# Kernel optimization log

Hardware: AMD Instinct MI355X
Metric: run time of the kernel (lower is better)

## Reference

```python
import jax, jax.numpy as jnp
import numpy as np

N_NODES = 100000
N_EDGES = 1600000
N_GRAPHS = 512
F_IN, HID, EMB = 256, 64, 2


def gcn_layer(h, src, dst, W, b, n_nodes):
    # PyG GCNConv: h' = D^{-1/2} (A + I) D^{-1/2} (h W) + b
    h = h @ W  # [N, out]
    loop = jnp.arange(n_nodes)
    s = jnp.concatenate([src, loop])
    d = jnp.concatenate([dst, loop])
    deg = jax.ops.segment_sum(jnp.ones_like(d, dtype=h.dtype), d, num_segments=n_nodes)
    dinv = jnp.where(deg > 0, jax.lax.rsqrt(deg), 0.0)
    norm = dinv[s] * dinv[d]  # [E+N]
    msg = h[s] * norm[:, None]  # gather + scale
    return jax.ops.segment_sum(msg, d, num_segments=n_nodes) + b


def setup_inputs() -> dict:
    key = jax.random.key(0)
    k1, k2, k3, k4, k5, k6 = jax.random.split(key, 6)
    x = jax.random.normal(k1, (N_NODES, F_IN), dtype=jnp.float32)
    edge_index = jax.random.randint(k2, (2, N_EDGES), 0, N_NODES, dtype=jnp.int64)
    batch = jnp.sort(jax.random.randint(k3, (N_NODES,), 0, N_GRAPHS, dtype=jnp.int64))
    # Glorot-ish init for layer weights
    W1 = jax.random.normal(k4, (F_IN, HID), dtype=jnp.float32) / np.sqrt(F_IN)
    b1 = jnp.zeros((HID,), dtype=jnp.float32)
    W2 = jax.random.normal(k5, (HID, EMB), dtype=jnp.float32) / np.sqrt(HID)
    b2 = jnp.zeros((EMB,), dtype=jnp.float32)
    return {"x": x, "edge_index": edge_index, "batch": batch,
            "W1": W1, "b1": b1, "W2": W2, "b2": b2}


def reference(x, edge_index, batch, W1, b1, W2, b2):
    n = x.shape[0]
    src, dst = edge_index[0], edge_index[1]
    h = gcn_layer(x, src, dst, W1, b1, n)
    h = jax.nn.relu(h)
    h = gcn_layer(h, src, dst, W2, b2, n)
    # global_mean_pool over graph ids
    sums = jax.ops.segment_sum(h, batch, num_segments=N_GRAPHS)
    cnts = jax.ops.segment_sum(jnp.ones((n,), dtype=h.dtype), batch, num_segments=N_GRAPHS)
    return sums / jnp.maximum(cnts, 1.0)[:, None]
```

## Files before the change

kernel.cpp:

```cpp
#include <hip/hip_runtime.h>
#include <hip/hip_bf16.h>

#define FIN 256
#define HID 64
#define EMB 2
#define BKB 9
#define BKSZ 512
#define MAXBK 256
#define NBLK 256

typedef __bf16 bf16x8 __attribute__((ext_vector_type(8)));
typedef float  f32x16 __attribute__((ext_vector_type(16)));

static __device__ __forceinline__ unsigned short f2bf(float f) {
    union { float f; unsigned int u; } v; v.f = f;
    unsigned int u = v.u;
    unsigned int r = (u + 0x7fffu + ((u >> 16) & 1u)) >> 16;
    return (unsigned short)r;
}
static __device__ __forceinline__ float bf2f(unsigned short h) {
    union { unsigned int u; float f; } v; v.u = ((unsigned int)h) << 16;
    return v.f;
}

__global__ void zero_i_kernel(int* __restrict__ p, long n) {
    long i = (long)blockIdx.x * blockDim.x + threadIdx.x;
    if (i < n) p[i] = 0;
}

__global__ void scan1_kernel(const int* __restrict__ cnt, int* __restrict__ offs,
                             int* __restrict__ bsums, int M) {
    __shared__ int s[256];
    int tid = threadIdx.x;
    int i = blockIdx.x * 256 + tid;
    int v = (i < M) ? cnt[i] : 0;
    s[tid] = v;
    __syncthreads();
    for (int off = 1; off < 256; off <<= 1) {
        int t = (tid >= off) ? s[tid - off] : 0;
        __syncthreads();
        s[tid] += t;
        __syncthreads();
    }
    if (i < M) offs[i + 1] = s[tid];
    if (tid == 255) bsums[blockIdx.x] = s[255];
    if (i == 0) offs[0] = 0;
}

__global__ void scan2_kernel(int* __restrict__ bsums, int NB) {
    __shared__ int s[512];
    int tid = threadIdx.x;
    s[tid] = (tid < NB) ? bsums[tid] : 0;
    __syncthreads();
    for (int off = 1; off < 512; off <<= 1) {
        int t = (tid >= off) ? s[tid - off] : 0;
        __syncthreads();
        s[tid] += t;
        __syncthreads();
    }
    if (tid < NB) bsums[tid] = s[tid];
}

__global__ void scan3_kernel(int* __restrict__ offs, const int* __restrict__ bsums, int M) {
    int i = blockIdx.x * 256 + threadIdx.x;
    if (i < M && blockIdx.x > 0) offs[i + 1] += bsums[blockIdx.x - 1];
}

__global__ __launch_bounds__(256) void bin_hist_kernel(
        const int* __restrict__ dst, int* __restrict__ counts, int E, int chunk, int NBK) {
    __shared__ int hist[MAXBK];
    int tid = threadIdx.x;
    for (int b = tid; b < NBK; b += 256) hist[b] = 0;
    __syncthreads();
    int e0 = blockIdx.x * chunk, e1 = min(e0 + chunk, E);
    for (int i = e0 + tid; i < e1; i += 256) atomicAdd(&hist[dst[i] >> BKB], 1);
    __syncthreads();
    for (int b = tid; b < NBK; b += 256) counts[b * gridDim.x + blockIdx.x] = hist[b];
}

__global__ __launch_bounds__(256) void bin_scatter_kernel(
        const int* __restrict__ src, const int* __restrict__ dst,
        const int* __restrict__ offs, unsigned* __restrict__ ebuf,
        int E, int chunk, int NBK) {
    __shared__ int cur[MAXBK];
    int tid = threadIdx.x;
    for (int b = tid; b < NBK; b += 256) cur[b] = offs[b * gridDim.x + blockIdx.x];
    __syncthreads();
    int e0 = blockIdx.x * chunk, e1 = min(e0 + chunk, E);
    for (int i = e0 + tid; i < e1; i += 256) {
        int s = src[i], d = dst[i];
        int b = d >> BKB;
        int pos = atomicAdd(&cur[b], 1);
        ebuf[pos] = ((unsigned)s << BKB) | (unsigned)(d & (BKSZ - 1));
    }
}

__global__ __launch_bounds__(256) void build_kernel(
        const unsigned* __restrict__ ebuf, const int* __restrict__ offs,
        int* __restrict__ rowptr, float* __restrict__ dinv, int* __restrict__ csr,
        int N, int E) {
    __shared__ int hist[BKSZ];
    __shared__ int scanb[256];
    __shared__ int cur[BKSZ];
    const int b = blockIdx.x, tid = threadIdx.x;
    const int r0 = offs[b * NBLK];
    const int r1 = offs[(b + 1) * NBLK];
    const int nb0 = b * BKSZ;

    hist[tid] = 0; hist[tid + 256] = 0;
    __syncthreads();
    for (int i = r0 + tid; i < r1; i += 256)
        atomicAdd(&hist[ebuf[i] & (BKSZ - 1u)], 1);
    __syncthreads();

    int h0 = hist[2 * tid], h1 = hist[2 * tid + 1];
    if (nb0 + 2 * tid < N)     dinv[nb0 + 2 * tid]     = rsqrtf((float)h0 + 1.f);
    if (nb0 + 2 * tid + 1 < N) dinv[nb0 + 2 * tid + 1] = rsqrtf((float)h1 + 1.f);
    scanb[tid] = h0 + h1;
    __syncthreads();
    for (int off = 1; off < 256; off <<= 1) {
        int t = (tid >= off) ? scanb[tid - off] : 0;
        __syncthreads();
        scanb[tid] += t;
        __syncthreads();
    }
    int base0 = scanb[tid] - (h0 + h1);
    int o0 = base0, o1 = base0 + h0;
    cur[2 * tid] = o0; cur[2 * tid + 1] = o1;
    if (nb0 + 2 * tid < N)     rowptr[nb0 + 2 * tid]     = r0 + o0;
    if (nb0 + 2 * tid + 1 < N) rowptr[nb0 + 2 * tid + 1] = r0 + o1;
    if (nb0 + BKSZ >= N && tid == 0) rowptr[N] = E;
    __syncthreads();
    for (int i = r0 + tid; i < r1; i += 256) {
        unsigned u = ebuf[i];
        int loc = (int)(u & (BKSZ - 1u));
        int p = atomicAdd(&cur[loc], 1);
        csr[r0 + p] = (int)(u >> BKB);
    }
}

__global__ __launch_bounds__(256) void gemm1_kernel(
        const float* __restrict__ x, const float* __restrict__ W,
        const float* __restrict__ dinv, unsigned short* __restrict__ h1b, int N) {
    __shared__ __align__(16) __bf16 A_hi[2 * 4 * 64 * 8];
    __shared__ __align__(16) __bf16 A_lo[2 * 4 * 64 * 8];
    __shared__ __align__(16) __bf16 B_hi[2 * 4 * 64 * 8];
    __shared__ __align__(16) __bf16 B_lo[2 * 4 * 64 * 8];

    const int tid = threadIdx.x;
    const int base = blockIdx.x * 64;
    const int w = tid >> 6;
    const int l = tid & 63;
    const int mg = w >> 1, ng = w & 1;

    f32x16 acc = {};

    const int r  = tid & 63;
    const int ks = tid >> 6;
    const int rl = r & 31, rh = r >> 5;

    for (int ch = 0; ch < 4; ++ch) {
        const int ck0 = ch * 64;
        __syncthreads();
        {
            int row = base + r;
            float f[16];
            if (row < N) {
                const float* xp = &x[(size_t)row * FIN + ck0 + ks * 16];
                float4 v0 = *(const float4*)(xp + 0);
                float4 v1 = *(const float4*)(xp + 4);
                float4 v2 = *(const float4*)(xp + 8);
                float4 v3 = *(const float4*)(xp + 12);
                f[0]=v0.x; f[1]=v0.y; f[2]=v0.z; f[3]=v0.w;
                f[4]=v1.x; f[5]=v1.y; f[6]=v1.z; f[7]=v1.w;
                f[8]=v2.x; f[9]=v2.y; f[10]=v2.z; f[11]=v2.w;
                f[12]=v3.x; f[13]=v3.y; f[14]=v3.z; f[15]=v3.w;
            } else {
                #pragma unroll
                for (int q = 0; q < 16; ++q) f[q] = 0.f;
            }
            bf16x8 ha, hb, la, lb;
            #pragma unroll
            for (int q = 0; q < 8; ++q) {
                __bf16 h0 = (__bf16)f[q];
                ha[q] = h0; la[q] = (__bf16)(f[q] - (float)h0);
                __bf16 h1v = (__bf16)f[q + 8];
                hb[q] = h1v; lb[q] = (__bf16)(f[q + 8] - (float)h1v);
            }
            int ra = ((rh * 4 + ks) * 64 + rl) * 8;
            int rb = ((rh * 4 + ks) * 64 + 32 + rl) * 8;
            *(bf16x8*)&A_hi[ra] = ha; *(bf16x8*)&A_hi[rb] = hb;
            *(bf16x8*)&A_lo[ra] = la; *(bf16x8*)&A_lo[rb] = lb;
        }
        {
            const float* wp = &W[(size_t)(ck0 + ks * 16) * HID + r];
            float f[16];
            #pragma unroll
            for (int q = 0; q < 16; ++q) f[q] = wp[q * HID];
            bf16x8 ha, hb, la, lb;
            #pragma unroll
            for (int q = 0; q < 8; ++q) {
                __bf16 h0 = (__bf16)f[q];
                ha[q] = h0; la[q] = (__bf16)(f[q] - (float)h0);
                __bf16 h1v = (__bf16)f[q + 8];
                hb[q] = h1v; lb[q] = (__bf16)(f[q + 8] - (float)h1v);
            }
            int ra = ((rh * 4 + ks) * 64 + rl) * 8;
            int rb = ((rh * 4 + ks) * 64 + 32 + rl) * 8;
            *(bf16x8*)&B_hi[ra] = ha; *(bf16x8*)&B_hi[rb] = hb;
            *(bf16x8*)&B_lo[ra] = la; *(bf16x8*)&B_lo[rb] = lb;
        }
        __syncthreads();

        #pragma unroll
        for (int s = 0; s < 4; ++s) {
            bf16x8 a_h = *(const bf16x8*)&A_hi[((mg * 4 + s) * 64 + l) * 8];
            bf16x8 a_l = *(const bf16x8*)&A_lo[((mg * 4 + s) * 64 + l) * 8];
            bf16x8 b_h = *(const bf16x8*)&B_hi[((ng * 4 + s) * 64 + l) * 8];
            bf16x8 b_l = *(const bf16x8*)&B_lo[((ng * 4 + s) * 64 + l) * 8];
            acc = __builtin_amdgcn_mfma_f32_32x32x16_bf16(a_h, b_h, acc, 0, 0, 0);
            acc = __builtin_amdgcn_mfma_f32_32x32x16_bf16(a_h, b_l, acc, 0, 0, 0);
            acc = __builtin_amdgcn_mfma_f32_32x32x16_bf16(a_l, b_h, acc, 0, 0, 0);
        }
    }

    const int col = l & 31;
    const int rbase = 4 * (l >> 5);
    #pragma unroll
    for (int reg = 0; reg < 16; ++reg) {
        int row = (reg & 3) + 8 * (reg >> 2) + rbase;
        int node = base + mg * 32 + row;
        if (node < N)
            h1b[(size_t)node * HID + ng * 32 + col] = f2bf(acc[reg] * dinv[node]);
    }
}

__global__ __launch_bounds__(256) void agg1_layer2_kernel(
        const int* __restrict__ rowptr, const int* __restrict__ csr,
        const unsigned short* __restrict__ h1b,
        const float* __restrict__ dinv, const float* __restrict__ b1,
        const float* __restrict__ W2, float* __restrict__ h2, int N) {
    long t = (long)blockIdx.x * blockDim.x + threadIdx.x;
    int n = (int)(t >> 4);
    int li = threadIdx.x & 15;
    if (n >= N) return;
    const ushort4* h14 = (const ushort4*)h1b;

    float di = dinv[n];
    ushort4 sl = h14[(size_t)n * 16 + li];
    float v0 = bf2f(sl.x), v1 = bf2f(sl.y);
    float v2 = bf2f(sl.z), v3 = bf2f(sl.w);

    int j0 = rowptr[n], j1 = rowptr[n + 1];
    int j = j0;
    for (; j + 3 < j1; j += 4) {
        int s0 = csr[j], s1 = csr[j + 1], s2 = csr[j + 2], s3 = csr[j + 3];
        ushort4 g0 = h14[(size_t)s0 * 16 + li];
        ushort4 g1 = h14[(size_t)s1 * 16 + li];
        ushort4 g2 = h14[(size_t)s2 * 16 + li];
        ushort4 g3 = h14[(size_t)s3 * 16 + li];
        v0 += bf2f(g0.x) + bf2f(g1.x) + bf2f(g2.x) + bf2f(g3.x);
        v1 += bf2f(g0.y) + bf2f(g1.y) + bf2f(g2.y) + bf2f(g3.y);
        v2 += bf2f(g0.z) + bf2f(g1.z) + bf2f(g2.z) + bf2f(g3.z);
        v3 += bf2f(g0.w) + bf2f(g1.w) + bf2f(g2.w) + bf2f(g3.w);
    }
    for (; j < j1; ++j) {
        int s = csr[j];
        ushort4 g = h14[(size_t)s * 16 + li];
        v0 += bf2f(g.x); v1 += bf2f(g.y); v2 += bf2f(g.z); v3 += bf2f(g.w);
    }

    const float4 b4 = *(const float4*)&b1[li * 4];
    v0 = fmaxf(di * v0 + b4.x, 0.f); v1 = fmaxf(di * v1 + b4.y, 0.f);
    v2 = fmaxf(di * v2 + b4.z, 0.f); v3 = fmaxf(di * v3 + b4.w, 0.f);

    const float4* W24 = (const float4*)W2;
    float4 wa = W24[li * 2], wb = W24[li * 2 + 1];
    float r0 = v0 * wa.x + v1 * wa.z + v2 * wb.x + v3 * wb.z;
    float r1 = v0 * wa.y + v1 * wa.w + v2 * wb.y + v3 * wb.w;
    #pragma unroll
    for (int off = 1; off < 16; off <<= 1) {
        r0 += __shfl_xor(r0, off);
        r1 += __shfl_xor(r1, off);
    }
    if (li == 0) *(float2*)&h2[(size_t)n * EMB] = make_float2(r0 * di, r1 * di);
}

__global__ __launch_bounds__(256) void agg2_pool_kernel(
        const int* __restrict__ rowptr, const int* __restrict__ csr,
        const float* __restrict__ h2,
        const float* __restrict__ dinv, const float* __restrict__ b2,
        const int* __restrict__ batch,
        float* __restrict__ sums, float* __restrict__ cntf, int N) {
    int n = blockIdx.x * blockDim.x + threadIdx.x;
    int lane = threadIdx.x & 63;
    const float2* h2v = (const float2*)h2;
    float v0 = 0.f, v1 = 0.f, c = 0.f;
    int g = -1;
    if (n < N) {
        float di = dinv[n];
        float2 hs = h2v[n];
        v0 = hs.x; v1 = hs.y;
        int j0 = rowptr[n], j1 = rowptr[n + 1];
        int j = j0;
        for (; j + 3 < j1; j += 4) {
            int s0 = csr[j], s1 = csr[j + 1], s2 = csr[j + 2], s3 = csr[j + 3];
            float2 a = h2v[s0], b = h2v[s1], cc = h2v[s2], d = h2v[s3];
            v0 += a.x + b.x + cc.x + d.x;
            v1 += a.y + b.y + cc.y + d.y;
        }
        for (; j < j1; ++j) {
            float2 hv = h2v[csr[j]];
            v0 += hv.x; v1 += hv.y;
        }
        v0 = di * v0 + b2[0];
        v1 = di * v1 + b2[1];
        g = batch[n];
        c = 1.f;
    }
    #pragma unroll
    for (int off = 1; off < 64; off <<= 1) {
        int gg = __shfl_up(g, off);
        float t0 = __shfl_up(v0, off);
        float t1 = __shfl_up(v1, off);
        float tc = __shfl_up(c, off);
        if (lane >= off && gg == g) { v0 += t0; v1 += t1; c += tc; }
    }
    int gn = __shfl_down(g, 1);
    if (g >= 0 && (lane == 63 || gn != g)) {
        atomicAdd(&sums[g * EMB + 0], v0);
        atomicAdd(&sums[g * EMB + 1], v1);
        atomicAdd(&cntf[g], c);
    }
}

__global__ void final_kernel(const float* __restrict__ sums, const float* __restrict__ cntf,
                             float* __restrict__ out, int G) {
    int g = blockIdx.x * blockDim.x + threadIdx.x;
    if (g >= G) return;
    float c = fmaxf(cntf[g], 1.0f);
    out[g * EMB + 0] = sums[g * EMB + 0] / c;
    out[g * EMB + 1] = sums[g * EMB + 1] / c;
}

extern "C" void kernel_launch(void* const* d_in, const int* in_sizes, int n_in,
                              void* d_out, int out_size, void* d_ws, size_t ws_size,
                              hipStream_t stream) {
    const float* x     = (const float*)d_in[0];
    const int*   ei    = (const int*)d_in[1];
    const int*   batch = (const int*)d_in[2];
    const float* W1    = (const float*)d_in[3];
    const float* b1    = (const float*)d_in[4];
    const float* W2    = (const float*)d_in[5];
    const float* b2    = (const float*)d_in[6];
    float* out = (float*)d_out;

    const int N = in_sizes[0] / FIN;
    const int E = in_sizes[1] / 2;
    const int G = out_size / EMB;
    const int* src = ei;
    const int* dst = ei + E;

    const int NBK = (N + BKSZ - 1) / BKSZ;
    const int M = NBK * NBLK;
    const int NBs = (M + 255) / 256;
    const int chunk = (E + NBLK - 1) / NBLK;

    char* p = (char*)d_ws;
    auto take = [&](size_t bytes) { char* r = p; p += (bytes + 15) & ~(size_t)15; return r; };
    int*      counts = (int*)take(sizeof(int) * M);
    int*      offs   = (int*)take(sizeof(int) * (M + 1));
    int*      bsums  = (int*)take(sizeof(int) * 512);
    unsigned* ebuf   = (unsigned*)take(sizeof(unsigned) * E);
    int*      csr    = (int*)take(sizeof(int) * E);
    int*      rowptr = (int*)take(sizeof(int) * (N + 1));
    float*    dinv   = (float*)take(sizeof(float) * N);
    unsigned short* h1b = (unsigned short*)take(sizeof(unsigned short) * (size_t)N * HID);
    float*    h2     = (float*)take(sizeof(float) * (size_t)N * EMB);
    float*    sums   = (float*)take(sizeof(float) * G * EMB);
    float*    cntf   = (float*)take(sizeof(float) * G);

    zero_i_kernel<<<(3 * G + 255) / 256, 256, 0, stream>>>((int*)sums, 3L * G);
    bin_hist_kernel<<<NBLK, 256, 0, stream>>>(dst, counts, E, chunk, NBK);
    scan1_kernel<<<NBs, 256, 0, stream>>>(counts, offs, bsums, M);
    scan2_kernel<<<1, 512, 0, stream>>>(bsums, NBs);
    scan3_kernel<<<NBs, 256, 0, stream>>>(offs, bsums, M);
    bin_scatter_kernel<<<NBLK, 256, 0, stream>>>(src, dst, offs, ebuf, E, chunk, NBK);
    build_kernel<<<NBK, 256, 0, stream>>>(ebuf, offs, rowptr, dinv, csr, N, E);
    gemm1_kernel<<<(N + 63) / 64, 256, 0, stream>>>(x, W1, dinv, h1b, N);
    agg1_layer2_kernel<<<(int)(((long)N * 16 + 255) / 256), 256, 0, stream>>>(
        rowptr, csr, h1b, dinv, b1, W2, h2, N);
    agg2_pool_kernel<<<(N + 255) / 256, 256, 0, stream>>>(
        rowptr, csr, h2, dinv, b2, batch, sums, cntf, N);
    final_kernel<<<(G + 255) / 256, 256, 0, stream>>>(sums, cntf, out, G);
}
```

Baseline: 304.0 us.

## Split layer-1 aggregation into four column-plane passes for cache locality

The GEMM output is written as four column planes of 16 features each. The neighbour aggregation now runs four times, once per plane, writing fp32 partial sums, and a separate finish kernel applies bias, ReLU and the W2 projection. The aim is to make each pass's gather working set small enough to stay in cache instead of randomly gathering full 128-byte rows. In exchange, the CSR indices are read four times, an extra fp32 intermediate buffer is written and read, and there are more kernel launches.

Result: slower. 326.8 us (+7.5%).

```diff
diff --git a/kernel.cpp b/kernel.cpp
--- a/kernel.cpp
+++ b/kernel.cpp
@@ -141,7 +141,7 @@
 
 __global__ __launch_bounds__(256) void gemm1_kernel(
         const float* __restrict__ x, const float* __restrict__ W,
-        const float* __restrict__ dinv, unsigned short* __restrict__ h1b, int N) {
+        const float* __restrict__ dinv, unsigned short* __restrict__ h1p, int N) {
     __shared__ __align__(16) __bf16 A_hi[2 * 4 * 64 * 8];
     __shared__ __align__(16) __bf16 A_lo[2 * 4 * 64 * 8];
     __shared__ __align__(16) __bf16 B_hi[2 * 4 * 64 * 8];
@@ -226,62 +226,76 @@
 
     const int col = l & 31;
     const int rbase = 4 * (l >> 5);
+    const int plane = ng * 2 + (col >> 4);
+    const int c16 = col & 15;
     #pragma unroll
     for (int reg = 0; reg < 16; ++reg) {
         int row = (reg & 3) + 8 * (reg >> 2) + rbase;
         int node = base + mg * 32 + row;
         if (node < N)
-            h1b[(size_t)node * HID + ng * 32 + col] = f2bf(acc[reg] * dinv[node]);
-    }
-}
-
-__global__ __launch_bounds__(256) void agg1_layer2_kernel(
+            h1p[((size_t)plane * N + node) * 16 + c16] = f2bf(acc[reg] * dinv[node]);
+    }
+}
+
+__global__ __launch_bounds__(256) void agg1_pass_kernel(
         const int* __restrict__ rowptr, const int* __restrict__ csr,
-        const unsigned short* __restrict__ h1b,
+        const unsigned short* __restrict__ h1plane,
+        float* __restrict__ pagg,
+        int N) {
+    long t = (long)blockIdx.x * blockDim.x + threadIdx.x;
+    int n = (int)(t >> 2);
+    int li = (int)(t & 3);
+    if (n >= N) return;
+    const ushort4* hp = (const ushort4*)h1plane;
+
+    ushort4 sl = hp[(size_t)n * 4 + li];
+    float v0 = bf2f(sl.x), v1 = bf2f(sl.y), v2 = bf2f(sl.z), v3 = bf2f(sl.w);
+
+    int j0 = rowptr[n], j1 = rowptr[n + 1];
+    int j = j0;
+    for (; j + 3 < j1; j += 4) {
+        int s0 = csr[j], s1 = csr[j + 1], s2 = csr[j + 2], s3 = csr[j + 3];
+        ushort4 g0 = hp[(size_t)s0 * 4 + li];
+        ushort4 g1 = hp[(size_t)s1 * 4 + li];
+        ushort4 g2 = hp[(size_t)s2 * 4 + li];
+        ushort4 g3 = hp[(size_t)s3 * 4 + li];
+        v0 += bf2f(g0.x) + bf2f(g1.x) + bf2f(g2.x) + bf2f(g3.x);
+        v1 += bf2f(g0.y) + bf2f(g1.y) + bf2f(g2.y) + bf2f(g3.y);
+        v2 += bf2f(g0.z) + bf2f(g1.z) + bf2f(g2.z) + bf2f(g3.z);
+        v3 += bf2f(g0.w) + bf2f(g1.w) + bf2f(g2.w) + bf2f(g3.w);
+    }
+    for (; j < j1; ++j) {
+        ushort4 g = hp[(size_t)csr[j] * 4 + li];
+        v0 += bf2f(g.x); v1 += bf2f(g.y); v2 += bf2f(g.z); v3 += bf2f(g.w);
+    }
+    *(float4*)&pagg[((size_t)n * 4 + li) * 4] = make_float4(v0, v1, v2, v3);
+}
+
+__global__ __launch_bounds__(256) void finish1_kernel(
+        const float* __restrict__ pagg,
         const float* __restrict__ dinv, const float* __restrict__ b1,
         const float* __restrict__ W2, float* __restrict__ h2, int N) {
     long t = (long)blockIdx.x * blockDim.x + threadIdx.x;
     int n = (int)(t >> 4);
     int li = threadIdx.x & 15;
     if (n >= N) return;
-    const ushort4* h14 = (const ushort4*)h1b;
-
+    int plane = li >> 2, off = (li & 3) * 4;
+    float4 v = *(const float4*)&pagg[((size_t)plane * N + n) * 16 + off];
     float di = dinv[n];
-    ushort4 sl = h14[(size_t)n * 16 + li];
-    float v0 = bf2f(sl.x), v1 = bf2f(sl.y);
-    float v2 = bf2f(sl.z), v3 = bf2f(sl.w);
-
-    int j0 = rowptr[n], j1 = rowptr[n + 1];
-    int j = j0;
-    for (; j + 3 < j1; j += 4) {
-        int s0 = csr[j], s1 = csr[j + 1], s2 = csr[j + 2], s3 = csr[j + 3];
-        ushort4 g0 = h14[(size_t)s0 * 16 + li];
-        ushort4 g1 = h14[(size_t)s1 * 16 + li];
-        ushort4 g2 = h14[(size_t)s2 * 16 + li];
-        ushort4 g3 = h14[(size_t)s3 * 16 + li];
-        v0 += bf2f(g0.x) + bf2f(g1.x) + bf2f(g2.x) + bf2f(g3.x);
-        v1 += bf2f(g0.y) + bf2f(g1.y) + bf2f(g2.y) + bf2f(g3.y);
-        v2 += bf2f(g0.z) + bf2f(g1.z) + bf2f(g2.z) + bf2f(g3.z);
-        v3 += bf2f(g0.w) + bf2f(g1.w) + bf2f(g2.w) + bf2f(g3.w);
-    }
-    for (; j < j1; ++j) {
-        int s = csr[j];
-        ushort4 g = h14[(size_t)s * 16 + li];
-        v0 += bf2f(g.x); v1 += bf2f(g.y); v2 += bf2f(g.z); v3 += bf2f(g.w);
-    }
-
     const float4 b4 = *(const float4*)&b1[li * 4];
-    v0 = fmaxf(di * v0 + b4.x, 0.f); v1 = fmaxf(di * v1 + b4.y, 0.f);
-    v2 = fmaxf(di * v2 + b4.z, 0.f); v3 = fmaxf(di * v3 + b4.w, 0.f);
+    float v0 = fmaxf(di * v.x + b4.x, 0.f);
+    float v1 = fmaxf(di * v.y + b4.y, 0.f);
+    float v2 = fmaxf(di * v.z + b4.z, 0.f);
+    float v3 = fmaxf(di * v.w + b4.w, 0.f);
 
     const float4* W24 = (const float4*)W2;
     float4 wa = W24[li * 2], wb = W24[li * 2 + 1];
     float r0 = v0 * wa.x + v1 * wa.z + v2 * wb.x + v3 * wb.z;
     float r1 = v0 * wa.y + v1 * wa.w + v2 * wb.y + v3 * wb.w;
     #pragma unroll
-    for (int off = 1; off < 16; off <<= 1) {
-        r0 += __shfl_xor(r0, off);
-        r1 += __shfl_xor(r1, off);
+    for (int o = 1; o < 16; o <<= 1) {
+        r0 += __shfl_xor(r0, o);
+        r1 += __shfl_xor(r1, o);
     }
     if (li == 0) *(float2*)&h2[(size_t)n * EMB] = make_float2(r0 * di, r1 * di);
 }
@@ -375,7 +389,8 @@
     int*      csr    = (int*)take(sizeof(int) * E);
     int*      rowptr = (int*)take(sizeof(int) * (N + 1));
     float*    dinv   = (float*)take(sizeof(float) * N);
-    unsigned short* h1b = (unsigned short*)take(sizeof(unsigned short) * (size_t)N * HID);
+    unsigned short* h1p = (unsigned short*)take(sizeof(unsigned short) * (size_t)N * HID);
+    float*    pagg   = (float*)take(sizeof(float) * (size_t)N * HID);
     float*    h2     = (float*)take(sizeof(float) * (size_t)N * EMB);
     float*    sums   = (float*)take(sizeof(float) * G * EMB);
     float*    cntf   = (float*)take(sizeof(float) * G);
@@ -387,9 +402,16 @@
     scan3_kernel<<<NBs, 256, 0, stream>>>(offs, bsums, M);
     bin_scatter_kernel<<<NBLK, 256, 0, stream>>>(src, dst, offs, ebuf, E, chunk, NBK);
     build_kernel<<<NBK, 256, 0, stream>>>(ebuf, offs, rowptr, dinv, csr, N, E);
-    gemm1_kernel<<<(N + 63) / 64, 256, 0, stream>>>(x, W1, dinv, h1b, N);
-    agg1_layer2_kernel<<<(int)(((long)N * 16 + 255) / 256), 256, 0, stream>>>(
-        rowptr, csr, h1b, dinv, b1, W2, h2, N);
+    gemm1_kernel<<<(N + 63) / 64, 256, 0, stream>>>(x, W1, dinv, h1p, N);
+    {
+        int blocks = (int)(((long)N * 4 + 255) / 256);
+        for (int pl = 0; pl < 4; ++pl) {
+            agg1_pass_kernel<<<blocks, 256, 0, stream>>>(
+                rowptr, csr, h1p + (size_t)pl * N * 16, pagg + (size_t)pl * N * 16, N);
+        }
+        finish1_kernel<<<(int)(((long)N * 16 + 255) / 256), 256, 0, stream>>>(
+            pagg, dinv, b1, W2, h2, N);
+    }
     agg2_pool_kernel<<<(N + 255) / 256, 256, 0, stream>>>(
         rowptr, csr, h2, dinv, b2, batch, sums, cntf, N);
     final_kernel<<<(G + 255) / 256, 256, 0, stream>>>(sums, cntf, out, G);
```
